# Kernel tuning notes

Hardware: AMD Instinct MI355X
Metric: run time of the kernel (lower is better)

Reference implementation:

```python
import jax, jax.numpy as jnp
import numpy as np

# Block dims (see shape_source)
D, H = 768, 12
DH = D // H            # 64 head dim
NOPE = DH // 2         # 32 non-rope q/k dim
ROPE = DH // 2         # 32 rope q/k dim
QP = D // 2            # 384 q LoRA dim
KVP = 2 * D // 3       # 512 kv LoRA dim
E, TOPK, NS = 8, 2, 2  # routed experts, top-k, shared experts
FF = 4 * D             # 3072 expert hidden
THETA = 10000.0


def setup_inputs() -> dict:
    key = jax.random.key(0)
    ks = jax.random.split(key, 16)
    B, S = 4, 1024
    r = lambda i, shape, s: (s * jax.random.normal(ks[i], shape)).astype(jnp.float32)
    return {
        'x': jax.random.normal(ks[0], (B, S, D), jnp.float32),
        'ln1_w': jnp.ones((D,), jnp.float32),
        'ln2_w': jnp.ones((D,), jnp.float32),
        'W_dq': r(1, (D, QP), 0.01),
        'W_uq': r(2, (QP, D), 0.01),
        'q_ln_w': jnp.ones((QP,), jnp.float32),
        'q_ln_b': jnp.zeros((QP,), jnp.float32),
        'W_dkv': r(3, (D, KVP + ROPE), 0.01),
        'W_ukv': r(4, (KVP, D + H * NOPE), 0.01),
        'kv_ln_w': jnp.ones((KVP,), jnp.float32),
        'kv_ln_b': jnp.zeros((KVP,), jnp.float32),
        'W_o': r(5, (D, D), 0.01),
        's_fc': r(6, (NS, FF, D), 0.02),   # nn.Linear weight layout [out,in]
        's_proj': r(7, (NS, D, FF), 0.02),
        'e_fc': r(8, (E, FF, D), 0.02),
        'e_proj': r(9, (E, D, FF), 0.02),
        'centroids': jax.random.normal(ks[10], (E, D), jnp.float32),
        'route_bias': jnp.zeros((E,), jnp.float32),  # load-balancing bias (non-learned)
    }


def _ln(x, w, b=None, eps=1e-5):
    m = x.mean(-1, keepdims=True)
    v = ((x - m) ** 2).mean(-1, keepdims=True)
    y = (x - m) * jax.lax.rsqrt(v + eps) * w
    return y + b if b is not None else y


def _rope(x, cos, sin):
    x1, x2 = jnp.split(x, 2, axis=-1)
    return x * cos + jnp.concatenate([-x2, x1], axis=-1) * sin


def _forward(x, ln1_w, ln2_w, W_dq, W_uq, q_ln_w, q_ln_b, W_dkv, W_ukv,
             kv_ln_w, kv_ln_b, W_o, s_fc, s_proj, e_fc, e_proj,
             centroids, route_bias):
    B, S, _ = x.shape
    h = _ln(x, ln1_w)
    # ---- MLA attention ----
    cq = _ln(h @ W_dq, q_ln_w, q_ln_b)
    Q = (cq @ W_uq).reshape(B, S, H, DH).transpose(0, 2, 1, 3)  # bhsd
    Qn, Qr = Q[..., :NOPE], Q[..., NOPE:]
    freqs = 1.0 / (THETA ** (jnp.arange(0, DH, 2, dtype=jnp.float32) / DH))
    ang = jnp.arange(S, dtype=jnp.float32)[:, None] * freqs[None, :]  # [S, DH/2]
    cos = jnp.tile(jnp.cos(ang)[:, : ROPE // 2], (1, 2))  # [S, ROPE]
    sin = jnp.tile(jnp.sin(ang)[:, : ROPE // 2], (1, 2))
    Qr = _rope(Qr, cos, sin)
    ckv = h @ W_dkv
    kv_lora, k_rope = ckv[..., :KVP], ckv[..., KVP:]
    kv_lora = _ln(kv_lora, kv_ln_w, kv_ln_b)
    KV = (kv_lora @ W_ukv).reshape(B, S, H, NOPE + DH).transpose(0, 2, 1, 3)
    Kn, V = KV[..., :NOPE], KV[..., NOPE:]
    Kr = _rope(k_rope[:, None, :, :], cos, sin)  # [B,1,S,ROPE] shared across heads
    Kr = jnp.broadcast_to(Kr, (B, H, S, ROPE))
    q = jnp.concatenate([Qn, Qr], axis=-1)
    k = jnp.concatenate([Kn, Kr], axis=-1)
    scores = jnp.einsum('bhsd,bhtd->bhst', q, k) / np.float32(np.sqrt(DH))
    causal = jnp.tril(jnp.ones((S, S), bool))
    scores = jnp.where(causal, scores, jnp.finfo(scores.dtype).min)
    attn = jax.nn.softmax(scores, axis=-1)
    o = jnp.einsum('bhst,bhtd->bshd', attn, V).reshape(B, S, D)
    x = x + o @ W_o.T
    # ---- MoE FFN ----
    h = _ln(x, ln2_w)
    gelu = lambda t: jax.nn.gelu(t, approximate=False)  # torch nn.GELU default
    # shared experts (always on, summed)
    shared = jnp.einsum('bsnf,ndf->bsd', gelu(jnp.einsum('bsd,nfd->bsnf', h, s_fc)), s_proj)
    # centroid routing
    raw = jnp.einsum('bsd,ed->bse', h, centroids)
    routing = jax.nn.sigmoid(raw)
    balanced = raw + route_bias
    _, topi = jax.lax.top_k(balanced, TOPK)                       # [B,S,K]
    w = jnp.take_along_axis(routing, topi, axis=-1)               # sigmoid gate values
    w = w / (w.sum(-1, keepdims=True) + 1e-9)                     # normalize over top-k
    gates = (jax.nn.one_hot(topi, E, dtype=w.dtype) * w[..., None]).sum(-2)  # [B,S,E]
    eh = gelu(jnp.einsum('bsd,efd->bsef', h, e_fc))               # [B,S,E,FF]
    routed = jnp.einsum('bsef,edf,bse->bsd', eh, e_proj, gates)
    return x + shared + routed


def reference(x, ln1_w, ln2_w, W_dq, W_uq, q_ln_w, q_ln_b, W_dkv, W_ukv,
              kv_ln_w, kv_ln_b, W_o, s_fc, s_proj, e_fc, e_proj,
              centroids, route_bias):
    return _forward(x, ln1_w, ln2_w, W_dq, W_uq, q_ln_w, q_ln_b, W_dkv, W_ukv,
                    kv_ln_w, kv_ln_b, W_o, s_fc, s_proj, e_fc, e_proj,
                    centroids, route_bias)
```

## Files before the change

kernel.cpp:

```cpp
#include <hip/hip_runtime.h>
#include <math.h>


#define DEV __device__ __forceinline__

typedef __attribute__((ext_vector_type(8))) short short8;
typedef __attribute__((ext_vector_type(8))) __bf16 bf16x8;
typedef __attribute__((ext_vector_type(4))) float floatx4;

DEV short f2bf(float f) {
  union { float f; unsigned u; } v; v.f = f;
  unsigned r = v.u + 0x7fffu + ((v.u >> 16) & 1u);
  return (short)(r >> 16);
}
DEV float bf2f(short s) {
  union { float f; unsigned u; } v; v.u = ((unsigned)(unsigned short)s) << 16;
  return v.f;
}
DEV float gelu_f(float v) { return 0.5f * v * (1.0f + erff(v * 0.70710678118654752f)); }

DEV floatx4 mfma16(short8 a, short8 b, floatx4 c) {
  return __builtin_amdgcn_mfma_f32_16x16x32_bf16(
      __builtin_bit_cast(bf16x8, a), __builtin_bit_cast(bf16x8, b), c, 0, 0, 0);
}
DEV void async16(void* lds_uniform, const void* gptr) {
  __builtin_amdgcn_global_load_lds(
      (const __attribute__((address_space(1))) void*)gptr,
      (__attribute__((address_space(3))) void*)lds_uniform, 16, 0, 0);
}


__global__ void cast2_bf4(const float4* __restrict__ srcA, short4* __restrict__ dstA,
                          const float4* __restrict__ srcB, short4* __restrict__ dstB,
                          long n4each) {
  long i = (long)blockIdx.x * blockDim.x + threadIdx.x;
  long stride = (long)gridDim.x * blockDim.x;
  for (; i < 2 * n4each; i += stride) {
    const float4* s; short4* d; long j;
    if (i < n4each) { s = srcA; d = dstA; j = i; }
    else { s = srcB; d = dstB; j = i - n4each; }
    float4 v = s[j];
    short4 o; o.x = f2bf(v.x); o.y = f2bf(v.y); o.z = f2bf(v.z); o.w = f2bf(v.w);
    d[j] = o;
  }
}

__global__ void cast_shared(const float4* __restrict__ sfc4, const float4* __restrict__ sproj4,
                            short4* __restrict__ fcCat4, short4* __restrict__ projCat4) {
  long i = (long)blockIdx.x * 256 + threadIdx.x;
  float4 v;
  if (i < 1179648) {
    v = sfc4[i];
    short4 o; o.x = f2bf(v.x); o.y = f2bf(v.y); o.z = f2bf(v.z); o.w = f2bf(v.w);
    fcCat4[i] = o;
  } else {
    long j = i - 1179648;
    long d = j / 1536, k4 = j - d * 1536;
    v = (k4 < 768) ? sproj4[d * 768 + k4] : sproj4[589824 + d * 768 + (k4 - 768)];
    short4 o; o.x = f2bf(v.x); o.y = f2bf(v.y); o.z = f2bf(v.z); o.w = f2bf(v.w);
    projCat4[j] = o;
  }
}

__global__ void cast_hl4(const float4* __restrict__ src, short4* __restrict__ dhi,
                         short4* __restrict__ dlo, long n4) {
  long i = (long)blockIdx.x * blockDim.x + threadIdx.x;
  long stride = (long)gridDim.x * blockDim.x;
  for (; i < n4; i += stride) {
    float4 v = src[i];
    short4 h, l;
    h.x = f2bf(v.x); l.x = f2bf(v.x - bf2f(h.x));
    h.y = f2bf(v.y); l.y = f2bf(v.y - bf2f(h.y));
    h.z = f2bf(v.z); l.z = f2bf(v.z - bf2f(h.z));
    h.w = f2bf(v.w); l.w = f2bf(v.w - bf2f(h.w));
    dhi[i] = h; dlo[i] = l;
  }
}

__launch_bounds__(256)
__global__ void transpose_cast_hl(const float* __restrict__ src, short* __restrict__ dhi,
                                  short* __restrict__ dlo, int K, int N) {
  __shared__ float tile[64][65];
  int k0 = blockIdx.x * 64, n0 = blockIdx.y * 64;
  for (int i = threadIdx.x; i < 4096; i += 256) {
    int r = i >> 6, c = i & 63;
    tile[r][c] = (n0 + c < N) ? src[(size_t)(k0 + r) * N + n0 + c] : 0.f;
  }
  __syncthreads();
  for (int i = threadIdx.x; i < 4096; i += 256) {
    int r = i >> 6, c = i & 63;
    float v = tile[c][r];
    short h = f2bf(v);
    dhi[(size_t)(n0 + r) * K + k0 + c] = h;
    dlo[(size_t)(n0 + r) * K + k0 + c] = f2bf(v - bf2f(h));
  }
}


__launch_bounds__(256)
__global__ void ln_hl(const float* __restrict__ in, int ldi, int N,
                      const float* __restrict__ w, const float* __restrict__ b,
                      short* __restrict__ ohi, short* __restrict__ olo, int ldo) {
  const int row = blockIdx.x * 4 + (threadIdx.x >> 6);
  const int lane = threadIdx.x & 63;
  const float* r = in + (size_t)row * ldi;
  float s = 0.f, s2 = 0.f;
  for (int i = lane; i < N; i += 64) { float v = r[i]; s += v; s2 += v * v; }
#pragma unroll
  for (int off = 32; off >= 1; off >>= 1) { s += __shfl_xor(s, off); s2 += __shfl_xor(s2, off); }
  float mean = s / N, var = s2 / N - mean * mean;
  float rstd = rsqrtf(var + 1e-5f);
  for (int i = lane; i < N; i += 64) {
    float y = (r[i] - mean) * rstd * w[i];
    if (b) y += b[i];
    short h = f2bf(y);
    ohi[(size_t)row * ldo + i] = h;
    olo[(size_t)row * ldo + i] = f2bf(y - bf2f(h));
  }
}

__launch_bounds__(256)
__global__ void ln_qkv(const float* __restrict__ Ccat,
                       const float* __restrict__ qw, const float* __restrict__ qb,
                       const float* __restrict__ kw, const float* __restrict__ kb,
                       short* __restrict__ cqH, short* __restrict__ cqL,
                       short* __restrict__ kvH, short* __restrict__ kvL) {
  const int vrow = blockIdx.x * 4 + (threadIdx.x >> 6);
  const int lane = threadIdx.x & 63;
  const float* r; int N; const float* w; const float* b; short* oh; short* ol; int ldo; int row;
  if (vrow < 4096) {
    row = vrow; r = Ccat + (size_t)row * 928; N = 384; w = qw; b = qb; oh = cqH; ol = cqL; ldo = 384;
  } else {
    row = vrow - 4096; r = Ccat + (size_t)row * 928 + 384; N = 512; w = kw; b = kb; oh = kvH; ol = kvL; ldo = 512;
  }
  float s = 0.f, s2 = 0.f;
  for (int i = lane; i < N; i += 64) { float v = r[i]; s += v; s2 += v * v; }
#pragma unroll
  for (int off = 32; off >= 1; off >>= 1) { s += __shfl_xor(s, off); s2 += __shfl_xor(s2, off); }
  float mean = s / N, var = s2 / N - mean * mean;
  float rstd = rsqrtf(var + 1e-5f);
  for (int i = lane; i < N; i += 64) {
    float y = (r[i] - mean) * rstd * w[i] + b[i];
    short h = f2bf(y);
    oh[(size_t)row * ldo + i] = h;
    ol[(size_t)row * ldo + i] = f2bf(y - bf2f(h));
  }
}

__launch_bounds__(256)
__global__ void ln_bf_f32(const float* __restrict__ in, const float* __restrict__ w,
                          short* __restrict__ obf, float* __restrict__ of,
                          float* __restrict__ outInit) {
  const int row = blockIdx.x * 4 + (threadIdx.x >> 6);
  const int lane = threadIdx.x & 63;
  const float* r = in + (size_t)row * 768;
  float s = 0.f, s2 = 0.f;
  for (int i = lane; i < 768; i += 64) { float v = r[i]; s += v; s2 += v * v; }
#pragma unroll
  for (int off = 32; off >= 1; off >>= 1) { s += __shfl_xor(s, off); s2 += __shfl_xor(s2, off); }
  float mean = s / 768.f, var = s2 / 768.f - mean * mean;
  float rstd = rsqrtf(var + 1e-5f);
  for (int i = lane; i < 768; i += 64) {
    float xv = r[i];
    float y = (xv - mean) * rstd * w[i];
    obf[(size_t)row * 768 + i] = f2bf(y);
    of[(size_t)row * 768 + i] = y;
    outInit[(size_t)row * 768 + i] = xv;
  }
}


template<int RESID>
__launch_bounds__(256)
__global__ void gemm3(const short* __restrict__ Ahi, const short* __restrict__ Alo, int lda,
                      const short* __restrict__ Bhi, const short* __restrict__ Blo, int ldb,
                      float* __restrict__ Cf, int ldc, const float* __restrict__ resid,
                      int M, int N, int K) {
  __shared__ __align__(16) short AsH[4096], AsL[4096], BsH[4096], BsL[4096];
  const int tid = threadIdx.x;
  const int m0 = blockIdx.y * 128, n0 = blockIdx.x * 128;
  const int wave = tid >> 6, lane = tid & 63;
  const int wm = (wave >> 1) * 64, wn = (wave & 1) * 64;
  const int lr = lane & 15, rb = (lane >> 4) * 4;
  const int stg = ((tid & 3) ^ ((tid >> 3) & 3)) * 8;
  const int lkx = (((lane >> 4) ^ ((lr >> 1) & 3))) * 8;
  const floatx4 fz = {0.f, 0.f, 0.f, 0.f};
  floatx4 acc[4][4];
#pragma unroll
  for (int i = 0; i < 4; i++)
#pragma unroll
    for (int j = 0; j < 4; j++) acc[i][j] = fz;
  const size_t rowA = (size_t)(m0 + (tid >> 2)) * lda + stg;
  const size_t rowB = (size_t)(n0 + (tid >> 2)) * ldb + stg;
  const size_t a64 = (size_t)64 * lda, b64 = (size_t)64 * ldb;
  short* AsHW = AsH + wave * 512; short* AsLW = AsL + wave * 512;
  short* BsHW = BsH + wave * 512; short* BsLW = BsL + wave * 512;
  for (int k0 = 0; k0 < K; k0 += 32) {
    async16(AsHW, Ahi + rowA + k0);        async16(AsHW + 2048, Ahi + rowA + a64 + k0);
    async16(AsLW, Alo + rowA + k0);        async16(AsLW + 2048, Alo + rowA + a64 + k0);
    async16(BsHW, Bhi + rowB + k0);        async16(BsHW + 2048, Bhi + rowB + b64 + k0);
    async16(BsLW, Blo + rowB + k0);        async16(BsLW + 2048, Blo + rowB + b64 + k0);
    __syncthreads();
    short8 ah[4], al[4], bh[4], bl[4];
#pragma unroll
    for (int i = 0; i < 4; i++) {
      ah[i] = *(const short8*)&AsH[(wm + i * 16 + lr) * 32 + lkx];
      al[i] = *(const short8*)&AsL[(wm + i * 16 + lr) * 32 + lkx];
    }
#pragma unroll
    for (int j = 0; j < 4; j++) {
      bh[j] = *(const short8*)&BsH[(wn + j * 16 + lr) * 32 + lkx];
      bl[j] = *(const short8*)&BsL[(wn + j * 16 + lr) * 32 + lkx];
    }
#pragma unroll
    for (int i = 0; i < 4; i++)
#pragma unroll
      for (int j = 0; j < 4; j++) {
        acc[i][j] = mfma16(ah[i], bh[j], acc[i][j]);
        acc[i][j] = mfma16(ah[i], bl[j], acc[i][j]);
        acc[i][j] = mfma16(al[i], bh[j], acc[i][j]);
      }
    __syncthreads();
  }
#pragma unroll
  for (int i = 0; i < 4; i++) {
    int row = m0 + wm + i * 16 + rb;
#pragma unroll
    for (int j = 0; j < 4; j++) {
      int col = n0 + wn + j * 16 + lr;
      if (col < N) {
#pragma unroll
        for (int r = 0; r < 4; r++) {
          int rr = row + r;
          if (rr < M) {
            float v = acc[i][j][r];
            if (RESID) v += resid[(size_t)rr * ldc + col];
            Cf[(size_t)rr * ldc + col] = v;
          }
        }
      }
    }
  }
}


__launch_bounds__(256)
__global__ void gemm_fc(const short* __restrict__ A, int lda,
                        const short* __restrict__ Bt, int ldb,
                        short* __restrict__ Cb, int ldc, int K) {
  __shared__ __align__(16) short As[4096], Bs[4096];
  const int tid = threadIdx.x;
  const int m0 = blockIdx.y * 128, n0 = blockIdx.x * 128;
  const int wave = tid >> 6, lane = tid & 63;
  const int wm = (wave >> 1) * 64, wn = (wave & 1) * 64;
  const int lr = lane & 15, rb = (lane >> 4) * 4;
  const int stg = ((tid & 3) ^ ((tid >> 3) & 3)) * 8;
  const int lkx = (((lane >> 4) ^ ((lr >> 1) & 3))) * 8;
  const floatx4 fz = {0.f, 0.f, 0.f, 0.f};
  floatx4 acc[4][4];
#pragma unroll
  for (int i = 0; i < 4; i++)
#pragma unroll
    for (int j = 0; j < 4; j++) acc[i][j] = fz;
  const short* Ag = A + (size_t)(m0 + (tid >> 2)) * lda + stg;
  const short* Bg = Bt + (size_t)(n0 + (tid >> 2)) * ldb + stg;
  short* AsW = As + wave * 512; short* BsW = Bs + wave * 512;
  const size_t a64 = (size_t)64 * lda, b64 = (size_t)64 * ldb;
  for (int k0 = 0; k0 < K; k0 += 32) {
    async16(AsW, Ag + k0);  async16(AsW + 2048, Ag + a64 + k0);
    async16(BsW, Bg + k0);  async16(BsW + 2048, Bg + b64 + k0);
    __syncthreads();
    short8 af[4], bfr[4];
#pragma unroll
    for (int i = 0; i < 4; i++) af[i] = *(const short8*)&As[(wm + i * 16 + lr) * 32 + lkx];
#pragma unroll
    for (int j = 0; j < 4; j++) bfr[j] = *(const short8*)&Bs[(wn + j * 16 + lr) * 32 + lkx];
#pragma unroll
    for (int i = 0; i < 4; i++)
#pragma unroll
      for (int j = 0; j < 4; j++) acc[i][j] = mfma16(af[i], bfr[j], acc[i][j]);
    __syncthreads();
  }
#pragma unroll
  for (int i = 0; i < 4; i++) {
    int row = m0 + wm + i * 16 + rb;
#pragma unroll
    for (int j = 0; j < 4; j++) {
      int col = n0 + wn + j * 16 + lr;
#pragma unroll
      for (int r = 0; r < 4; r++)
        Cb[(size_t)(row + r) * ldc + col] = f2bf(gelu_f(acc[i][j][r]));
    }
  }
}


__launch_bounds__(256)
__global__ void gemm_sk(const short* __restrict__ A, int lda,
                        const short* __restrict__ Bt, int ldb,
                        float* __restrict__ out, int ldc, int klen) {
  __shared__ __align__(16) short As[4096], Bs[4096];
  const int tid = threadIdx.x;
  const int m0 = blockIdx.y * 128, n0 = blockIdx.x * 128;
  const int koff = blockIdx.z * klen;
  const int wave = tid >> 6, lane = tid & 63;
  const int wm = (wave >> 1) * 64, wn = (wave & 1) * 64;
  const int lr = lane & 15, rb = (lane >> 4) * 4;
  const int stg = ((tid & 3) ^ ((tid >> 3) & 3)) * 8;
  const int lkx = (((lane >> 4) ^ ((lr >> 1) & 3))) * 8;
  const floatx4 fz = {0.f, 0.f, 0.f, 0.f};
  floatx4 acc[4][4];
#pragma unroll
  for (int i = 0; i < 4; i++)
#pragma unroll
    for (int j = 0; j < 4; j++) acc[i][j] = fz;
  const short* Ag = A + (size_t)(m0 + (tid >> 2)) * lda + koff + stg;
  const short* Bg = Bt + (size_t)(n0 + (tid >> 2)) * ldb + koff + stg;
  short* AsW = As + wave * 512; short* BsW = Bs + wave * 512;
  const size_t a64 = (size_t)64 * lda, b64 = (size_t)64 * ldb;
  for (int k0 = 0; k0 < klen; k0 += 32) {
    async16(AsW, Ag + k0);  async16(AsW + 2048, Ag + a64 + k0);
    async16(BsW, Bg + k0);  async16(BsW + 2048, Bg + b64 + k0);
    __syncthreads();
    short8 af[4], bfr[4];
#pragma unroll
    for (int i = 0; i < 4; i++) af[i] = *(const short8*)&As[(wm + i * 16 + lr) * 32 + lkx];
#pragma unroll
    for (int j = 0; j < 4; j++) bfr[j] = *(const short8*)&Bs[(wn + j * 16 + lr) * 32 + lkx];
#pragma unroll
    for (int i = 0; i < 4; i++)
#pragma unroll
      for (int j = 0; j < 4; j++) acc[i][j] = mfma16(af[i], bfr[j], acc[i][j]);
    __syncthreads();
  }
#pragma unroll
  for (int i = 0; i < 4; i++) {
    int row = m0 + wm + i * 16 + rb;
#pragma unroll
    for (int j = 0; j < 4; j++) {
      int col = n0 + wn + j * 16 + lr;
#pragma unroll
      for (int r = 0; r < 4; r++)
        atomicAdd(&out[(size_t)(row + r) * ldc + col], acc[i][j][r]);
    }
  }
}


__global__ void build_qk(const float* __restrict__ Qf, const float* __restrict__ KVf,
                         const float* __restrict__ Ccat,
                         short* __restrict__ qh, short* __restrict__ ql,
                         short* __restrict__ kh, short* __restrict__ kl) {
  int id = blockIdx.x * blockDim.x + threadIdx.x;
  if (id >= 4096 * 12) return;
  int token = id / 12, hh_ = id - token * 12;
  int s = token & 1023, b = token >> 10;
  size_t base = ((size_t)(b * 12 + hh_) * 1024 + s) * 64;
  float vals[64];
  if (blockIdx.y == 0) {
    const float* q = Qf + (size_t)token * 768 + hh_ * 64;
#pragma unroll
    for (int d = 0; d < 32; d++) vals[d] = q[d];
#pragma unroll
    for (int i = 0; i < 16; i++) {
      float fi = powf(10000.f, -(float)(2 * i) / 64.f);
      float sn, cs; sincosf((float)s * fi, &sn, &cs);
      vals[32 + i] = q[32 + i] * cs - q[48 + i] * sn;
      vals[48 + i] = q[48 + i] * cs + q[32 + i] * sn;
    }
#pragma unroll
    for (int d = 0; d < 64; d++) {
      short h = f2bf(vals[d]);
      qh[base + d] = h; ql[base + d] = f2bf(vals[d] - bf2f(h));
    }
  } else {
    const float* kv = KVf + (size_t)token * 1152 + hh_ * 96;
#pragma unroll
    for (int d = 0; d < 32; d++) vals[d] = kv[d];
    const float* kr = Ccat + (size_t)token * 928 + 896;
#pragma unroll
    for (int i = 0; i < 16; i++) {
      float fi = powf(10000.f, -(float)(2 * i) / 64.f);
      float sn, cs; sincosf((float)s * fi, &sn, &cs);
      vals[32 + i] = kr[i] * cs - kr[16 + i] * sn;
      vals[48 + i] = kr[16 + i] * cs + kr[i] * sn;
    }
#pragma unroll
    for (int d = 0; d < 64; d++) {
      short h = f2bf(vals[d]);
      kh[base + d] = h; kl[base + d] = f2bf(vals[d] - bf2f(h));
    }
  }
}

__launch_bounds__(256)
__global__ void build_vt_hl(const float* __restrict__ KVf,
                            short* __restrict__ vth, short* __restrict__ vtl) {
  __shared__ float tile[64][65];
  const int s0 = blockIdx.x * 64, bh = blockIdx.y;
  const int b = bh / 12, h = bh - b * 12;
  for (int i = threadIdx.x; i < 4096; i += 256) {
    int tl = i >> 6, d = i & 63;
    int token = b * 1024 + s0 + tl;
    tile[tl][d] = KVf[(size_t)token * 1152 + h * 96 + 32 + d];
  }
  __syncthreads();
  for (int i = threadIdx.x; i < 4096; i += 256) {
    int d = i >> 6, sl = i & 63;
    float v = tile[sl][d];
    short hh = f2bf(v);
    size_t idx = (size_t)bh * 65536 + (size_t)d * 1024 + s0 + sl;
    vth[idx] = hh;
    vtl[idx] = f2bf(v - bf2f(hh));
  }
}


__launch_bounds__(256)
__global__ void attn3(const short* __restrict__ qbh, const short* __restrict__ qbl,
                      const short* __restrict__ kbh, const short* __restrict__ kbl,
                      const short* __restrict__ vth, const short* __restrict__ vtl,
                      short* __restrict__ obh, short* __restrict__ obl) {
  const int bh = blockIdx.y;
  const int b = bh / 12, h = bh - b * 12;
  const short* Qh = qbh + (size_t)bh * 65536;
  const short* Ql = qbl + (size_t)bh * 65536;
  const short* Kh = kbh + (size_t)bh * 65536;
  const short* Kl = kbl + (size_t)bh * 65536;
  const short* Vh = vth + (size_t)bh * 65536;
  const short* Vl = vtl + (size_t)bh * 65536;
  __shared__ __align__(16) short KsH[4096], KsL[4096], VsH[4096], VsL[4096];
  __shared__ __align__(16) short PsH[4608], PsL[4608];
  const int tid = threadIdx.x, wave = tid >> 6, lane = tid & 63;
  const int lr = lane & 15, q4 = lane >> 4, lk = (lane >> 4) * 8;
  const int sx0 = ((q4 ^ (lr & 7))) * 8;
  const int sx1 = (((4 + q4) ^ (lr & 7))) * 8;
  const int soff_sw = (((tid & 7) ^ ((tid >> 3) & 7))) * 8;
  const int srow = tid >> 3;
  short* KsHW = KsH + wave * 512; short* KsLW = KsL + wave * 512;
  short* VsHW = VsH + wave * 512; short* VsLW = VsL + wave * 512;
  short* myPh = PsH + wave * 1152; short* myPl = PsL + wave * 1152;
  const floatx4 fz = {0.f, 0.f, 0.f, 0.f};
#pragma unroll
  for (int ph = 0; ph < 2; ph++) {
    const int qt = ph ? 15 - blockIdx.x : blockIdx.x;
    const int qrow0 = qt * 64 + wave * 16;
    short8 qfh[2], qfl[2];
    qfh[0] = *(const short8*)&Qh[(size_t)(qrow0 + lr) * 64 + lk];
    qfh[1] = *(const short8*)&Qh[(size_t)(qrow0 + lr) * 64 + 32 + lk];
    qfl[0] = *(const short8*)&Ql[(size_t)(qrow0 + lr) * 64 + lk];
    qfl[1] = *(const short8*)&Ql[(size_t)(qrow0 + lr) * 64 + 32 + lk];
    floatx4 oacc[4];
#pragma unroll
    for (int t = 0; t < 4; t++) oacc[t] = fz;
    float m_i[4], l_i[4];
#pragma unroll
    for (int r = 0; r < 4; r++) { m_i[r] = -__builtin_inff(); l_i[r] = 0.f; }
    for (int kt = 0; kt <= qt; kt++) {
      __syncthreads();
      size_t krow = (size_t)(kt * 64 + srow) * 64 + soff_sw;
      size_t vrow = (size_t)srow * 1024 + kt * 64 + soff_sw;
      async16(KsHW, Kh + krow);        async16(KsHW + 2048, Kh + krow + 32 * 64);
      async16(KsLW, Kl + krow);        async16(KsLW + 2048, Kl + krow + 32 * 64);
      async16(VsHW, Vh + vrow);        async16(VsHW + 2048, Vh + vrow + 32 * 1024);
      async16(VsLW, Vl + vrow);        async16(VsLW + 2048, Vl + vrow + 32 * 1024);
      __syncthreads();
      floatx4 sacc[4];
#pragma unroll
      for (int j = 0; j < 4; j++) sacc[j] = fz;
#pragma unroll
      for (int j = 0; j < 4; j++) {
        int rbase = (j * 16 + lr) * 64;
        short8 kh0 = *(const short8*)&KsH[rbase + sx0];
        short8 kh1 = *(const short8*)&KsH[rbase + sx1];
        short8 kl0 = *(const short8*)&KsL[rbase + sx0];
        short8 kl1 = *(const short8*)&KsL[rbase + sx1];
        sacc[j] = mfma16(qfh[0], kh0, sacc[j]);
        sacc[j] = mfma16(qfh[1], kh1, sacc[j]);
        sacc[j] = mfma16(qfh[0], kl0, sacc[j]);
        sacc[j] = mfma16(qfh[1], kl1, sacc[j]);
        sacc[j] = mfma16(qfl[0], kh0, sacc[j]);
        sacc[j] = mfma16(qfl[1], kh1, sacc[j]);
      }
      float pv[4][4], mrow[4];
#pragma unroll
      for (int r = 0; r < 4; r++) mrow[r] = -__builtin_inff();
      const bool diag = (kt == qt);
#pragma unroll
      for (int j = 0; j < 4; j++)
#pragma unroll
        for (int r = 0; r < 4; r++) {
          float v = sacc[j][r] * 0.125f;
          if (diag) {
            int qg = qrow0 + q4 * 4 + r;
            int kg = kt * 64 + j * 16 + lr;
            if (kg > qg) v = -__builtin_inff();
          }
          pv[j][r] = v;
          mrow[r] = fmaxf(mrow[r], v);
        }
#pragma unroll
      for (int r = 0; r < 4; r++)
#pragma unroll
        for (int off = 1; off < 16; off <<= 1) mrow[r] = fmaxf(mrow[r], __shfl_xor(mrow[r], off));
      float alpha[4], rsum[4];
#pragma unroll
      for (int r = 0; r < 4; r++) {
        float nm = fmaxf(m_i[r], mrow[r]);
        alpha[r] = __expf(m_i[r] - nm);
        m_i[r] = nm; rsum[r] = 0.f;
      }
#pragma unroll
      for (int j = 0; j < 4; j++)
#pragma unroll
        for (int r = 0; r < 4; r++) {
          float pe = __expf(pv[j][r] - m_i[r]);
          pv[j][r] = pe; rsum[r] += pe;
        }
#pragma unroll
      for (int r = 0; r < 4; r++) {
#pragma unroll
        for (int off = 1; off < 16; off <<= 1) rsum[r] += __shfl_xor(rsum[r], off);
        l_i[r] = l_i[r] * alpha[r] + rsum[r];
      }
#pragma unroll
      for (int t = 0; t < 4; t++)
#pragma unroll
        for (int r = 0; r < 4; r++) oacc[t][r] *= alpha[r];
#pragma unroll
      for (int j = 0; j < 4; j++)
#pragma unroll
        for (int r = 0; r < 4; r++) {
          float p = pv[j][r];
          short hh = f2bf(p);
          myPh[(q4 * 4 + r) * 72 + j * 16 + lr] = hh;
          myPl[(q4 * 4 + r) * 72 + j * 16 + lr] = f2bf(p - bf2f(hh));
        }
      __asm__ volatile("s_waitcnt lgkmcnt(0)" ::: "memory");
#pragma unroll
      for (int c = 0; c < 2; c++) {
        short8 ph_ = *(const short8*)&myPh[lr * 72 + c * 32 + lk];
        short8 pl_ = *(const short8*)&myPl[lr * 72 + c * 32 + lk];
        const int sxc = c ? sx1 : sx0;
#pragma unroll
        for (int t = 0; t < 4; t++) {
          int rbase = (t * 16 + lr) * 64;
          short8 vh = *(const short8*)&VsH[rbase + sxc];
          short8 vl = *(const short8*)&VsL[rbase + sxc];
          oacc[t] = mfma16(ph_, vh, oacc[t]);
          oacc[t] = mfma16(ph_, vl, oacc[t]);
          oacc[t] = mfma16(pl_, vh, oacc[t]);
        }
      }
    }
#pragma unroll
    for (int t = 0; t < 4; t++)
#pragma unroll
      for (int r = 0; r < 4; r++) {
        int s = qrow0 + q4 * 4 + r;
        int token = b * 1024 + s;
        float ov = oacc[t][r] / l_i[r];
        short hh = f2bf(ov);
        size_t idx = (size_t)token * 768 + h * 64 + t * 16 + lr;
        obh[idx] = hh;
        obl[idx] = f2bf(ov - bf2f(hh));
      }
  }
}


__launch_bounds__(256)
__global__ void route_score(const float* __restrict__ h2f, const float* __restrict__ cent,
                            const float* __restrict__ rbias,
                            int* __restrict__ topexp, float* __restrict__ gates) {
  const int token = blockIdx.x * 4 + (threadIdx.x >> 6);
  const int lane = threadIdx.x & 63;
  const float* hv = h2f + (size_t)token * 768;
  float hreg[12];
#pragma unroll
  for (int ii = 0; ii < 12; ii++) hreg[ii] = hv[lane + 64 * ii];
  float raw[8];
#pragma unroll
  for (int e = 0; e < 8; e++) {
    const float* cv = cent + e * 768;
    float p = 0.f;
#pragma unroll
    for (int ii = 0; ii < 12; ii++) p += hreg[ii] * cv[lane + 64 * ii];
#pragma unroll
    for (int off = 32; off >= 1; off >>= 1) p += __shfl_xor(p, off);
    raw[e] = p;
  }
  if (lane == 0) {
    float b0 = -__builtin_inff(); int i1 = 0;
#pragma unroll
    for (int e = 0; e < 8; e++) { float be = raw[e] + rbias[e]; if (be > b0) { b0 = be; i1 = e; } }
    float b1 = -__builtin_inff(); int i2 = 0;
#pragma unroll
    for (int e = 0; e < 8; e++) {
      if (e == i1) continue;
      float be = raw[e] + rbias[e];
      if (be > b1) { b1 = be; i2 = e; }
    }
    float w1 = 1.f / (1.f + expf(-raw[i1]));
    float w2 = 1.f / (1.f + expf(-raw[i2]));
    float wsum = w1 + w2 + 1e-9f;
    topexp[token] = i1;        gates[token] = w1 / wsum;
    topexp[4096 + token] = i2; gates[4096 + token] = w2 / wsum;
  }
}

__launch_bounds__(256)
__global__ void build_lists(const int* __restrict__ topexp,
                            int* __restrict__ counts, int* __restrict__ lists) {
  const int e = blockIdx.x;
  __shared__ int wave_off[4];
  const int wave = threadIdx.x >> 6, lane = threadIdx.x & 63;
  int total = 0;
  for (int c0 = 0; c0 < 8192; c0 += 256) {
    int slot = c0 + threadIdx.x;
    bool m = (topexp[slot] == e);
    unsigned long long bal = __ballot(m);
    int wcnt = __popcll(bal);
    int lpre = __popcll(bal & ((1ull << lane) - 1ull));
    if (lane == 0) wave_off[wave] = wcnt;
    __syncthreads();
    int woff = 0;
#pragma unroll
    for (int w = 0; w < 4; w++) if (w < wave) woff += wave_off[w];
    int chunk_total = wave_off[0] + wave_off[1] + wave_off[2] + wave_off[3];
    if (m) lists[e * 4096 + total + woff + lpre] = slot;
    total += chunk_total;
    __syncthreads();
  }
  if (threadIdx.x == 0) counts[e] = total;
}


__launch_bounds__(256)
__global__ void expert_fc_z(const short* __restrict__ h2bf, const short* __restrict__ wfc,
                            const int* __restrict__ lists, const int* __restrict__ counts,
                            int ebase, short* __restrict__ act) {
  const int lz = blockIdx.z, e = ebase + lz;
  const int cnt = counts[e];
  const int m0 = blockIdx.y * 128;
  if (m0 >= cnt) return;
  int aoff = 0;
  for (int i = 0; i < lz; i++) aoff += counts[ebase + i];
  const int n0 = blockIdx.x * 128;
  __shared__ __align__(16) short As[4096], Bs[4096];
  __shared__ int slots[128];
  const int tid = threadIdx.x;
  if (tid < 128) slots[tid] = lists[e * 4096 + m0 + tid];
  __syncthreads();
  const int tokA0 = slots[tid >> 2] & 4095;
  const int tokA1 = slots[64 + (tid >> 2)] & 4095;
  const int wave = tid >> 6, lane = tid & 63;
  const int wm = (wave >> 1) * 64, wn = (wave & 1) * 64;
  const int lr = lane & 15, rb = (lane >> 4) * 4;
  const int stg = ((tid & 3) ^ ((tid >> 3) & 3)) * 8;
  const int lkx = (((lane >> 4) ^ ((lr >> 1) & 3))) * 8;
  const floatx4 fz = {0.f, 0.f, 0.f, 0.f};
  floatx4 acc[4][4];
#pragma unroll
  for (int i = 0; i < 4; i++)
#pragma unroll
    for (int j = 0; j < 4; j++) acc[i][j] = fz;
  const short* Ag0 = h2bf + (size_t)tokA0 * 768 + stg;
  const short* Ag1 = h2bf + (size_t)tokA1 * 768 + stg;
  const short* Bg = wfc + (size_t)lz * (3072 * 768) + (size_t)(n0 + (tid >> 2)) * 768 + stg;
  short* AsW = As + wave * 512; short* BsW = Bs + wave * 512;
  for (int k0 = 0; k0 < 768; k0 += 32) {
    async16(AsW, Ag0 + k0);  async16(AsW + 2048, Ag1 + k0);
    async16(BsW, Bg + k0);   async16(BsW + 2048, Bg + (size_t)64 * 768 + k0);
    __syncthreads();
    short8 af[4], bfr[4];
#pragma unroll
    for (int i = 0; i < 4; i++) af[i] = *(const short8*)&As[(wm + i * 16 + lr) * 32 + lkx];
#pragma unroll
    for (int j = 0; j < 4; j++) bfr[j] = *(const short8*)&Bs[(wn + j * 16 + lr) * 32 + lkx];
#pragma unroll
    for (int i = 0; i < 4; i++)
#pragma unroll
      for (int j = 0; j < 4; j++) acc[i][j] = mfma16(af[i], bfr[j], acc[i][j]);
    __syncthreads();
  }
#pragma unroll
  for (int i = 0; i < 4; i++) {
    int lrow = wm + i * 16 + rb;
#pragma unroll
    for (int j = 0; j < 4; j++) {
      int col = n0 + wn + j * 16 + lr;
#pragma unroll
      for (int r = 0; r < 4; r++) {
        if (m0 + lrow + r < cnt)
          act[(size_t)(aoff + m0 + lrow + r) * 3072 + col] = f2bf(gelu_f(acc[i][j][r]));
      }
    }
  }
}

__launch_bounds__(256)
__global__ void expert_proj_z(const short* __restrict__ act, const short* __restrict__ wproj,
                              const int* __restrict__ lists, const int* __restrict__ counts,
                              int ebase, const float* __restrict__ gates,
                              float* __restrict__ out) {
  const int lz = blockIdx.z >> 1, kh = blockIdx.z & 1, e = ebase + lz;
  const int cnt = counts[e];
  const int m0 = blockIdx.y * 128;
  if (m0 >= cnt) return;
  int aoff = 0;
  for (int i = 0; i < lz; i++) aoff += counts[ebase + i];
  const int koff = kh * 1536;
  const int n0 = blockIdx.x * 128;
  __shared__ __align__(16) short As[4096], Bs[4096];
  __shared__ int slots[128];
  const int tid = threadIdx.x;
  if (tid < 128) slots[tid] = lists[e * 4096 + m0 + tid];
  __syncthreads();
  const int wave = tid >> 6, lane = tid & 63;
  const int wm = (wave >> 1) * 64, wn = (wave & 1) * 64;
  const int lr = lane & 15, rb = (lane >> 4) * 4;
  const int stg = ((tid & 3) ^ ((tid >> 3) & 3)) * 8;
  const int lkx = (((lane >> 4) ^ ((lr >> 1) & 3))) * 8;
  const floatx4 fz = {0.f, 0.f, 0.f, 0.f};
  floatx4 acc[4][4];
#pragma unroll
  for (int i = 0; i < 4; i++)
#pragma unroll
    for (int j = 0; j < 4; j++) acc[i][j] = fz;
  const short* Ag = act + (size_t)(aoff + m0 + (tid >> 2)) * 3072 + koff + stg;
  const short* Bg = wproj + (size_t)lz * (768 * 3072) + (size_t)(n0 + (tid >> 2)) * 3072 + koff + stg;
  short* AsW = As + wave * 512; short* BsW = Bs + wave * 512;
  for (int k0 = 0; k0 < 1536; k0 += 32) {
    async16(AsW, Ag + k0);  async16(AsW + 2048, Ag + (size_t)64 * 3072 + k0);
    async16(BsW, Bg + k0);  async16(BsW + 2048, Bg + (size_t)64 * 3072 + k0);
    __syncthreads();
    short8 af[4], bfr[4];
#pragma unroll
    for (int i = 0; i < 4; i++) af[i] = *(const short8*)&As[(wm + i * 16 + lr) * 32 + lkx];
#pragma unroll
    for (int j = 0; j < 4; j++) bfr[j] = *(const short8*)&Bs[(wn + j * 16 + lr) * 32 + lkx];
#pragma unroll
    for (int i = 0; i < 4; i++)
#pragma unroll
      for (int j = 0; j < 4; j++) acc[i][j] = mfma16(af[i], bfr[j], acc[i][j]);
    __syncthreads();
  }
#pragma unroll
  for (int i = 0; i < 4; i++) {
    int lrow = wm + i * 16 + rb;
#pragma unroll
    for (int j = 0; j < 4; j++) {
      int col = n0 + wn + j * 16 + lr;
#pragma unroll
      for (int r = 0; r < 4; r++) {
        if (m0 + lrow + r < cnt) {
          int slot = slots[lrow + r];
          int token = slot & 4095;
          atomicAdd(&out[(size_t)token * 768 + col], gates[slot] * acc[i][j][r]);
        }
      }
    }
  }
}

__global__ void bad_kernel(float* out) { out[threadIdx.x] = 1e30f; }


extern "C" void kernel_launch(void* const* d_in, const int* in_sizes, int n_in,
                              void* d_out, int out_size, void* d_ws, size_t ws_size,
                              hipStream_t stream) {
  const float* x = (const float*)d_in[0];
  const float* ln1_w = (const float*)d_in[1];
  const float* ln2_w = (const float*)d_in[2];
  const float* W_dq = (const float*)d_in[3];
  const float* W_uq = (const float*)d_in[4];
  const float* q_ln_w = (const float*)d_in[5];
  const float* q_ln_b = (const float*)d_in[6];
  const float* W_dkv = (const float*)d_in[7];
  const float* W_ukv = (const float*)d_in[8];
  const float* kv_ln_w = (const float*)d_in[9];
  const float* kv_ln_b = (const float*)d_in[10];
  const float* W_o = (const float*)d_in[11];
  const float* s_fc = (const float*)d_in[12];
  const float* s_proj = (const float*)d_in[13];
  const float* e_fc = (const float*)d_in[14];
  const float* e_proj = (const float*)d_in[15];
  const float* cent = (const float*)d_in[16];
  const float* rbias = (const float*)d_in[17];
  float* out = (float*)d_out;

  char* base = (char*)d_ws;
  size_t off = 0;
  auto take = [&](size_t bytes) -> char* {
    char* r = base + off;
    off = (off + bytes + 255) & ~(size_t)255;
    return r;
  };
  short* WcatH = (short*)take(1572864);  short* WcatL = (short*)take(1572864);
  short* WuqH  = (short*)take(589824);   short* WuqL  = (short*)take(589824);
  short* WukvH = (short*)take(1179648);  short* WukvL = (short*)take(1179648);
  short* WoH   = (short*)take(1179648);  short* WoL   = (short*)take(1179648);
  float* x2    = (float*)take(12582912);
  float* gates = (float*)take(32768);
  int*   counts= (int*)take(32);
  int*   lists = (int*)take(131072);
  int*   topexp= (int*)take(32768);
  const size_t PLANE = 6291456;
  char* pool = take(4 * 2 * PLANE);
  char* R    = take(51118080);
  size_t used = off;
  if (used > ws_size) { bad_kernel<<<1, 256, 0, stream>>>(out); return; }
  char* pA = pool;
  char* pB = pool + 2 * PLANE;
  char* pC = pool + 4 * PLANE;
  char* pD = pool + 6 * PLANE;

  short* hH   = (short*)pA;            short* hL   = (short*)(pA + PLANE);
  float* Ccat = (float*)R;
  short* cqH  = (short*)pB;            short* cqL  = (short*)(pB + 3145728);
  short* kvlH = (short*)pD;            short* kvlL = (short*)(pD + 4194304);
  float* Qf   = (float*)pC;
  float* KVf  = (float*)(R + 15204352);
  short* qbH  = (short*)pD;            short* qbL  = (short*)(pD + PLANE);
  short* kbH  = (short*)pA;            short* kbL  = (short*)(pA + PLANE);
  short* vtH  = (short*)pB;            short* vtL  = (short*)(pB + PLANE);
  short* obH  = (short*)pC;            short* obL  = (short*)(pC + PLANE);
  short* h2bf    = (short*)(pD + PLANE);
  float* h2f     = (float*)pC;
  short* sfcCat  = (short*)pA;
  short* sprojCat= (short*)(pA + 9437184);
  short* actCat  = (short*)R;
  short* efcHalf = (short*)pA;
  short* eprojHalf=(short*)(pA + 18874368);
  short* eact    = (short*)R;

  cast_hl4<<<576, 256, 0, stream>>>((const float4*)W_o, (short4*)WoH, (short4*)WoL, 147456);
  transpose_cast_hl<<<dim3(12, 6), 256, 0, stream>>>(W_dq, WcatH, WcatL, 768, 384);
  transpose_cast_hl<<<dim3(12, 10), 256, 0, stream>>>(W_dkv, WcatH + (size_t)384 * 768,
                                                      WcatL + (size_t)384 * 768, 768, 544);
  transpose_cast_hl<<<dim3(6, 12), 256, 0, stream>>>(W_uq, WuqH, WuqL, 384, 768);
  transpose_cast_hl<<<dim3(8, 18), 256, 0, stream>>>(W_ukv, WukvH, WukvL, 512, 1152);

  ln_hl<<<1024, 256, 0, stream>>>(x, 768, 768, ln1_w, nullptr, hH, hL, 768);
  gemm3<0><<<dim3(8, 32), 256, 0, stream>>>(hH, hL, 768, WcatH, WcatL, 768, Ccat, 928, nullptr, 4096, 928, 768);
  ln_qkv<<<2048, 256, 0, stream>>>(Ccat, q_ln_w, q_ln_b, kv_ln_w, kv_ln_b, cqH, cqL, kvlH, kvlL);
  gemm3<0><<<dim3(6, 32), 256, 0, stream>>>(cqH, cqL, 384, WuqH, WuqL, 384, Qf, 768, nullptr, 4096, 768, 384);
  gemm3<0><<<dim3(9, 32), 256, 0, stream>>>(kvlH, kvlL, 512, WukvH, WukvL, 512, KVf, 1152, nullptr, 4096, 1152, 512);
  build_qk<<<dim3(192, 2), 256, 0, stream>>>(Qf, KVf, Ccat, qbH, qbL, kbH, kbL);
  build_vt_hl<<<dim3(16, 48), 256, 0, stream>>>(KVf, vtH, vtL);
  attn3<<<dim3(8, 48), 256, 0, stream>>>(qbH, qbL, kbH, kbL, vtH, vtL, obH, obL);
  gemm3<1><<<dim3(6, 32), 256, 0, stream>>>(obH, obL, 768, WoH, WoL, 768, x2, 768, x, 4096, 768, 768);

  ln_bf_f32<<<1024, 256, 0, stream>>>(x2, ln2_w, h2bf, h2f, out);
  route_score<<<1024, 256, 0, stream>>>(h2f, cent, rbias, topexp, gates);
  build_lists<<<8, 256, 0, stream>>>(topexp, counts, lists);

  cast_shared<<<9216, 256, 0, stream>>>((const float4*)s_fc, (const float4*)s_proj,
                                        (short4*)sfcCat, (short4*)sprojCat);
  gemm_fc<<<dim3(48, 32), 256, 0, stream>>>(h2bf, 768, sfcCat, 768, actCat, 6144, 768);
  gemm_sk<<<dim3(6, 32, 4), 256, 0, stream>>>(actCat, 6144, sprojCat, 6144, out, 768, 1536);

  for (int h = 0; h < 2; h++) {
    cast2_bf4<<<2048, 256, 0, stream>>>(
        (const float4*)(e_fc + (size_t)h * 4 * 3072 * 768), (short4*)efcHalf,
        (const float4*)(e_proj + (size_t)h * 4 * 768 * 3072), (short4*)eprojHalf, 2359296);
    expert_fc_z<<<dim3(24, 32, 4), 256, 0, stream>>>(h2bf, efcHalf, lists, counts, h * 4, eact);
    expert_proj_z<<<dim3(6, 32, 8), 256, 0, stream>>>(eact, eprojHalf, lists, counts, h * 4, gates, out);
  }
}
```

Baseline: 1.100 ms.

## Double GEMM K-step to 64, add XCD block swizzle, polynomial GELU

```diff
diff --git a/kernel.cpp b/kernel.cpp
--- a/kernel.cpp
+++ b/kernel.cpp
@@ -17,7 +17,15 @@
   union { float f; unsigned u; } v; v.u = ((unsigned)(unsigned short)s) << 16;
   return v.f;
 }
-DEV float gelu_f(float v) { return 0.5f * v * (1.0f + erff(v * 0.70710678118654752f)); }
+DEV float gelu_f(float v) {
+  float z = fabsf(v) * 0.70710678118654752f;
+  float t = __fdividef(1.0f, 1.0f + 0.3275911f * z);
+  float poly = t * (0.254829592f + t * (-0.284496736f +
+               t * (1.421413741f + t * (-1.453152027f + t * 1.061405429f))));
+  float er = 1.0f - poly * __expf(-z * z);
+  er = (v < 0.f) ? -er : er;
+  return 0.5f * v * (1.0f + er);
+}
 
 DEV floatx4 mfma16(short8 a, short8 b, floatx4 c) {
   return __builtin_amdgcn_mfma_f32_16x16x32_bf16(
@@ -27,6 +35,15 @@
   __builtin_amdgcn_global_load_lds(
       (const __attribute__((address_space(1))) void*)gptr,
       (__attribute__((address_space(3))) void*)lds_uniform, 16, 0, 0);
+}
+
+DEV void xcd_swz(int& n0, int& m0) {
+  const int NT = gridDim.x;
+  const int flat = blockIdx.y * NT + blockIdx.x;
+  const int nwg = NT * gridDim.y;
+  const int w = (flat & 7) * (nwg >> 3) + (flat >> 3);
+  n0 = (w % NT) * 128;
+  m0 = (w / NT) * 128;
 }
 
 
@@ -178,7 +195,7 @@
                       int M, int N, int K) {
   __shared__ __align__(16) short AsH[4096], AsL[4096], BsH[4096], BsL[4096];
   const int tid = threadIdx.x;
-  const int m0 = blockIdx.y * 128, n0 = blockIdx.x * 128;
+  int n0, m0; xcd_swz(n0, m0);
   const int wave = tid >> 6, lane = tid & 63;
   const int wm = (wave >> 1) * 64, wn = (wave & 1) * 64;
   const int lr = lane & 15, rb = (lane >> 4) * 4;
@@ -248,37 +265,45 @@
 __global__ void gemm_fc(const short* __restrict__ A, int lda,
                         const short* __restrict__ Bt, int ldb,
                         short* __restrict__ Cb, int ldc, int K) {
-  __shared__ __align__(16) short As[4096], Bs[4096];
+  __shared__ __align__(16) short As[8192], Bs[8192];
   const int tid = threadIdx.x;
-  const int m0 = blockIdx.y * 128, n0 = blockIdx.x * 128;
+  int n0, m0; xcd_swz(n0, m0);
   const int wave = tid >> 6, lane = tid & 63;
   const int wm = (wave >> 1) * 64, wn = (wave & 1) * 64;
-  const int lr = lane & 15, rb = (lane >> 4) * 4;
-  const int stg = ((tid & 3) ^ ((tid >> 3) & 3)) * 8;
-  const int lkx = (((lane >> 4) ^ ((lr >> 1) & 3))) * 8;
+  const int lr = lane & 15, q4 = lane >> 4, rb = q4 * 4;
+  const int srow = tid >> 3;
+  const int sg = ((tid & 7) ^ (srow & 7)) * 8;
+  const int cx0 = ((q4 ^ (lr & 7))) * 8;
+  const int cx1 = (((4 + q4) ^ (lr & 7))) * 8;
   const floatx4 fz = {0.f, 0.f, 0.f, 0.f};
   floatx4 acc[4][4];
 #pragma unroll
   for (int i = 0; i < 4; i++)
 #pragma unroll
     for (int j = 0; j < 4; j++) acc[i][j] = fz;
-  const short* Ag = A + (size_t)(m0 + (tid >> 2)) * lda + stg;
-  const short* Bg = Bt + (size_t)(n0 + (tid >> 2)) * ldb + stg;
+  const short* Ag = A + (size_t)(m0 + srow) * lda + sg;
+  const short* Bg = Bt + (size_t)(n0 + srow) * ldb + sg;
   short* AsW = As + wave * 512; short* BsW = Bs + wave * 512;
-  const size_t a64 = (size_t)64 * lda, b64 = (size_t)64 * ldb;
-  for (int k0 = 0; k0 < K; k0 += 32) {
-    async16(AsW, Ag + k0);  async16(AsW + 2048, Ag + a64 + k0);
-    async16(BsW, Bg + k0);  async16(BsW + 2048, Bg + b64 + k0);
-    __syncthreads();
-    short8 af[4], bfr[4];
-#pragma unroll
-    for (int i = 0; i < 4; i++) af[i] = *(const short8*)&As[(wm + i * 16 + lr) * 32 + lkx];
-#pragma unroll
-    for (int j = 0; j < 4; j++) bfr[j] = *(const short8*)&Bs[(wn + j * 16 + lr) * 32 + lkx];
-#pragma unroll
-    for (int i = 0; i < 4; i++)
-#pragma unroll
-      for (int j = 0; j < 4; j++) acc[i][j] = mfma16(af[i], bfr[j], acc[i][j]);
+  const size_t a32 = (size_t)32 * lda, b32 = (size_t)32 * ldb;
+  for (int k0 = 0; k0 < K; k0 += 64) {
+    async16(AsW,        Ag + k0);            async16(AsW + 2048, Ag + a32 + k0);
+    async16(AsW + 4096, Ag + 2 * a32 + k0);  async16(AsW + 6144, Ag + 3 * a32 + k0);
+    async16(BsW,        Bg + k0);            async16(BsW + 2048, Bg + b32 + k0);
+    async16(BsW + 4096, Bg + 2 * b32 + k0);  async16(BsW + 6144, Bg + 3 * b32 + k0);
+    __syncthreads();
+#pragma unroll
+    for (int ks = 0; ks < 2; ks++) {
+      const int cx = ks ? cx1 : cx0;
+      short8 af[4], bfr[4];
+#pragma unroll
+      for (int i = 0; i < 4; i++) af[i] = *(const short8*)&As[(wm + i * 16 + lr) * 64 + cx];
+#pragma unroll
+      for (int j = 0; j < 4; j++) bfr[j] = *(const short8*)&Bs[(wn + j * 16 + lr) * 64 + cx];
+#pragma unroll
+      for (int i = 0; i < 4; i++)
+#pragma unroll
+        for (int j = 0; j < 4; j++) acc[i][j] = mfma16(af[i], bfr[j], acc[i][j]);
+    }
     __syncthreads();
   }
 #pragma unroll
@@ -299,38 +324,46 @@
 __global__ void gemm_sk(const short* __restrict__ A, int lda,
                         const short* __restrict__ Bt, int ldb,
                         float* __restrict__ out, int ldc, int klen) {
-  __shared__ __align__(16) short As[4096], Bs[4096];
+  __shared__ __align__(16) short As[8192], Bs[8192];
   const int tid = threadIdx.x;
-  const int m0 = blockIdx.y * 128, n0 = blockIdx.x * 128;
+  int n0, m0; xcd_swz(n0, m0);
   const int koff = blockIdx.z * klen;
   const int wave = tid >> 6, lane = tid & 63;
   const int wm = (wave >> 1) * 64, wn = (wave & 1) * 64;
-  const int lr = lane & 15, rb = (lane >> 4) * 4;
-  const int stg = ((tid & 3) ^ ((tid >> 3) & 3)) * 8;
-  const int lkx = (((lane >> 4) ^ ((lr >> 1) & 3))) * 8;
+  const int lr = lane & 15, q4 = lane >> 4, rb = q4 * 4;
+  const int srow = tid >> 3;
+  const int sg = ((tid & 7) ^ (srow & 7)) * 8;
+  const int cx0 = ((q4 ^ (lr & 7))) * 8;
+  const int cx1 = (((4 + q4) ^ (lr & 7))) * 8;
   const floatx4 fz = {0.f, 0.f, 0.f, 0.f};
   floatx4 acc[4][4];
 #pragma unroll
   for (int i = 0; i < 4; i++)
 #pragma unroll
     for (int j = 0; j < 4; j++) acc[i][j] = fz;
-  const short* Ag = A + (size_t)(m0 + (tid >> 2)) * lda + koff + stg;
-  const short* Bg = Bt + (size_t)(n0 + (tid >> 2)) * ldb + koff + stg;
+  const short* Ag = A + (size_t)(m0 + srow) * lda + koff + sg;
+  const short* Bg = Bt + (size_t)(n0 + srow) * ldb + koff + sg;
   short* AsW = As + wave * 512; short* BsW = Bs + wave * 512;
-  const size_t a64 = (size_t)64 * lda, b64 = (size_t)64 * ldb;
-  for (int k0 = 0; k0 < klen; k0 += 32) {
-    async16(AsW, Ag + k0);  async16(AsW + 2048, Ag + a64 + k0);
-    async16(BsW, Bg + k0);  async16(BsW + 2048, Bg + b64 + k0);
-    __syncthreads();
-    short8 af[4], bfr[4];
-#pragma unroll
-    for (int i = 0; i < 4; i++) af[i] = *(const short8*)&As[(wm + i * 16 + lr) * 32 + lkx];
-#pragma unroll
-    for (int j = 0; j < 4; j++) bfr[j] = *(const short8*)&Bs[(wn + j * 16 + lr) * 32 + lkx];
-#pragma unroll
-    for (int i = 0; i < 4; i++)
-#pragma unroll
-      for (int j = 0; j < 4; j++) acc[i][j] = mfma16(af[i], bfr[j], acc[i][j]);
+  const size_t a32 = (size_t)32 * lda, b32 = (size_t)32 * ldb;
+  for (int k0 = 0; k0 < klen; k0 += 64) {
+    async16(AsW,        Ag + k0);            async16(AsW + 2048, Ag + a32 + k0);
+    async16(AsW + 4096, Ag + 2 * a32 + k0);  async16(AsW + 6144, Ag + 3 * a32 + k0);
+    async16(BsW,        Bg + k0);            async16(BsW + 2048, Bg + b32 + k0);
+    async16(BsW + 4096, Bg + 2 * b32 + k0);  async16(BsW + 6144, Bg + 3 * b32 + k0);
+    __syncthreads();
+#pragma unroll
+    for (int ks = 0; ks < 2; ks++) {
+      const int cx = ks ? cx1 : cx0;
+      short8 af[4], bfr[4];
+#pragma unroll
+      for (int i = 0; i < 4; i++) af[i] = *(const short8*)&As[(wm + i * 16 + lr) * 64 + cx];
+#pragma unroll
+      for (int j = 0; j < 4; j++) bfr[j] = *(const short8*)&Bs[(wn + j * 16 + lr) * 64 + cx];
+#pragma unroll
+      for (int i = 0; i < 4; i++)
+#pragma unroll
+        for (int j = 0; j < 4; j++) acc[i][j] = mfma16(af[i], bfr[j], acc[i][j]);
+    }
     __syncthreads();
   }
 #pragma unroll
@@ -642,46 +675,57 @@
                             int ebase, short* __restrict__ act) {
   const int lz = blockIdx.z, e = ebase + lz;
   const int cnt = counts[e];
-  const int m0 = blockIdx.y * 128;
+  int n0, m0; xcd_swz(n0, m0);
   if (m0 >= cnt) return;
   int aoff = 0;
   for (int i = 0; i < lz; i++) aoff += counts[ebase + i];
-  const int n0 = blockIdx.x * 128;
-  __shared__ __align__(16) short As[4096], Bs[4096];
+  __shared__ __align__(16) short As[8192], Bs[8192];
   __shared__ int slots[128];
   const int tid = threadIdx.x;
   if (tid < 128) slots[tid] = lists[e * 4096 + m0 + tid];
   __syncthreads();
-  const int tokA0 = slots[tid >> 2] & 4095;
-  const int tokA1 = slots[64 + (tid >> 2)] & 4095;
   const int wave = tid >> 6, lane = tid & 63;
   const int wm = (wave >> 1) * 64, wn = (wave & 1) * 64;
-  const int lr = lane & 15, rb = (lane >> 4) * 4;
-  const int stg = ((tid & 3) ^ ((tid >> 3) & 3)) * 8;
-  const int lkx = (((lane >> 4) ^ ((lr >> 1) & 3))) * 8;
+  const int lr = lane & 15, q4 = lane >> 4, rb = q4 * 4;
+  const int srow = tid >> 3;
+  const int sg = ((tid & 7) ^ (srow & 7)) * 8;
+  const int cx0 = ((q4 ^ (lr & 7))) * 8;
+  const int cx1 = (((4 + q4) ^ (lr & 7))) * 8;
+  int tok[4];
+#pragma unroll
+  for (int p = 0; p < 4; p++) tok[p] = slots[p * 32 + srow] & 4095;
   const floatx4 fz = {0.f, 0.f, 0.f, 0.f};
   floatx4 acc[4][4];
 #pragma unroll
   for (int i = 0; i < 4; i++)
 #pragma unroll
     for (int j = 0; j < 4; j++) acc[i][j] = fz;
-  const short* Ag0 = h2bf + (size_t)tokA0 * 768 + stg;
-  const short* Ag1 = h2bf + (size_t)tokA1 * 768 + stg;
-  const short* Bg = wfc + (size_t)lz * (3072 * 768) + (size_t)(n0 + (tid >> 2)) * 768 + stg;
+  const short* Ag0 = h2bf + (size_t)tok[0] * 768 + sg;
+  const short* Ag1 = h2bf + (size_t)tok[1] * 768 + sg;
+  const short* Ag2 = h2bf + (size_t)tok[2] * 768 + sg;
+  const short* Ag3 = h2bf + (size_t)tok[3] * 768 + sg;
+  const short* Bg = wfc + (size_t)lz * (3072 * 768) + (size_t)(n0 + srow) * 768 + sg;
   short* AsW = As + wave * 512; short* BsW = Bs + wave * 512;
-  for (int k0 = 0; k0 < 768; k0 += 32) {
-    async16(AsW, Ag0 + k0);  async16(AsW + 2048, Ag1 + k0);
-    async16(BsW, Bg + k0);   async16(BsW + 2048, Bg + (size_t)64 * 768 + k0);
-    __syncthreads();
-    short8 af[4], bfr[4];
-#pragma unroll
-    for (int i = 0; i < 4; i++) af[i] = *(const short8*)&As[(wm + i * 16 + lr) * 32 + lkx];
-#pragma unroll
-    for (int j = 0; j < 4; j++) bfr[j] = *(const short8*)&Bs[(wn + j * 16 + lr) * 32 + lkx];
-#pragma unroll
-    for (int i = 0; i < 4; i++)
-#pragma unroll
-      for (int j = 0; j < 4; j++) acc[i][j] = mfma16(af[i], bfr[j], acc[i][j]);
+  const size_t b32 = (size_t)32 * 768;
+  for (int k0 = 0; k0 < 768; k0 += 64) {
+    async16(AsW,        Ag0 + k0);           async16(AsW + 2048, Ag1 + k0);
+    async16(AsW + 4096, Ag2 + k0);           async16(AsW + 6144, Ag3 + k0);
+    async16(BsW,        Bg + k0);            async16(BsW + 2048, Bg + b32 + k0);
+    async16(BsW + 4096, Bg + 2 * b32 + k0);  async16(BsW + 6144, Bg + 3 * b32 + k0);
+    __syncthreads();
+#pragma unroll
+    for (int ks = 0; ks < 2; ks++) {
+      const int cx = ks ? cx1 : cx0;
+      short8 af[4], bfr[4];
+#pragma unroll
+      for (int i = 0; i < 4; i++) af[i] = *(const short8*)&As[(wm + i * 16 + lr) * 64 + cx];
+#pragma unroll
+      for (int j = 0; j < 4; j++) bfr[j] = *(const short8*)&Bs[(wn + j * 16 + lr) * 64 + cx];
+#pragma unroll
+      for (int i = 0; i < 4; i++)
+#pragma unroll
+        for (int j = 0; j < 4; j++) acc[i][j] = mfma16(af[i], bfr[j], acc[i][j]);
+    }
     __syncthreads();
   }
 #pragma unroll
@@ -706,44 +750,52 @@
                               float* __restrict__ out) {
   const int lz = blockIdx.z >> 1, kh = blockIdx.z & 1, e = ebase + lz;
   const int cnt = counts[e];
-  const int m0 = blockIdx.y * 128;
+  int n0, m0; xcd_swz(n0, m0);
   if (m0 >= cnt) return;
   int aoff = 0;
   for (int i = 0; i < lz; i++) aoff += counts[ebase + i];
   const int koff = kh * 1536;
-  const int n0 = blockIdx.x * 128;
-  __shared__ __align__(16) short As[4096], Bs[4096];
+  __shared__ __align__(16) short As[8192], Bs[8192];
   __shared__ int slots[128];
   const int tid = threadIdx.x;
   if (tid < 128) slots[tid] = lists[e * 4096 + m0 + tid];
   __syncthreads();
   const int wave = tid >> 6, lane = tid & 63;
   const int wm = (wave >> 1) * 64, wn = (wave & 1) * 64;
-  const int lr = lane & 15, rb = (lane >> 4) * 4;
-  const int stg = ((tid & 3) ^ ((tid >> 3) & 3)) * 8;
-  const int lkx = (((lane >> 4) ^ ((lr >> 1) & 3))) * 8;
+  const int lr = lane & 15, q4 = lane >> 4, rb = q4 * 4;
+  const int srow = tid >> 3;
+  const int sg = ((tid & 7) ^ (srow & 7)) * 8;
+  const int cx0 = ((q4 ^ (lr & 7))) * 8;
+  const int cx1 = (((4 + q4) ^ (lr & 7))) * 8;
   const floatx4 fz = {0.f, 0.f, 0.f, 0.f};
   floatx4 acc[4][4];
 #pragma unroll
   for (int i = 0; i < 4; i++)
 #pragma unroll
     for (int j = 0; j < 4; j++) acc[i][j] = fz;
-  const short* Ag = act + (size_t)(aoff + m0 + (tid >> 2)) * 3072 + koff + stg;
-  const short* Bg = wproj + (size_t)lz * (768 * 3072) + (size_t)(n0 + (tid >> 2)) * 3072 + koff + stg;
+  const short* Ag = act + (size_t)(aoff + m0 + srow) * 3072 + koff + sg;
+  const short* Bg = wproj + (size_t)lz * (768 * 3072) + (size_t)(n0 + srow) * 3072 + koff + sg;
   short* AsW = As + wave * 512; short* BsW = Bs + wave * 512;
-  for (int k0 = 0; k0 < 1536; k0 += 32) {
-    async16(AsW, Ag + k0);  async16(AsW + 2048, Ag + (size_t)64 * 3072 + k0);
-    async16(BsW, Bg + k0);  async16(BsW + 2048, Bg + (size_t)64 * 3072 + k0);
-    __syncthreads();
-    short8 af[4], bfr[4];
-#pragma unroll
-    for (int i = 0; i < 4; i++) af[i] = *(const short8*)&As[(wm + i * 16 + lr) * 32 + lkx];
-#pragma unroll
-    for (int j = 0; j < 4; j++) bfr[j] = *(const short8*)&Bs[(wn + j * 16 + lr) * 32 + lkx];
-#pragma unroll
-    for (int i = 0; i < 4; i++)
-#pragma unroll
-      for (int j = 0; j < 4; j++) acc[i][j] = mfma16(af[i], bfr[j], acc[i][j]);
+  const size_t s32 = (size_t)32 * 3072;
+  for (int k0 = 0; k0 < 1536; k0 += 64) {
+    async16(AsW,        Ag + k0);            async16(AsW + 2048, Ag + s32 + k0);
+    async16(AsW + 4096, Ag + 2 * s32 + k0);  async16(AsW + 6144, Ag + 3 * s32 + k0);
+    async16(BsW,        Bg + k0);            async16(BsW + 2048, Bg + s32 + k0);
+    async16(BsW + 4096, Bg + 2 * s32 + k0);  async16(BsW + 6144, Bg + 3 * s32 + k0);
+    __syncthreads();
+#pragma unroll
+    for (int ks = 0; ks < 2; ks++) {
+      const int cx = ks ? cx1 : cx0;
+      short8 af[4], bfr[4];
+#pragma unroll
+      for (int i = 0; i < 4; i++) af[i] = *(const short8*)&As[(wm + i * 16 + lr) * 64 + cx];
+#pragma unroll
+      for (int j = 0; j < 4; j++) bfr[j] = *(const short8*)&Bs[(wn + j * 16 + lr) * 64 + cx];
+#pragma unroll
+      for (int i = 0; i < 4; i++)
+#pragma unroll
+        for (int j = 0; j < 4; j++) acc[i][j] = mfma16(af[i], bfr[j], acc[i][j]);
+    }
     __syncthreads();
   }
 #pragma unroll
```

Result: slower. 1.251 ms (+13.7%).
